# Optimization experiments

Measured on AMD Instinct MI355X. Metric: run time of the kernel, lower is better.

## Reference

```python
import jax, jax.numpy as jnp
import numpy as np

EPS = 1e-7

def _convolve(A, x, W, lw, lb):
    # A: [s,i,j,c+1] relation adjacency; keep first c=4 relations
    Ar = A[..., :-1]                               # [s,i,j,c]
    norm = 1.0 / (jnp.sum(Ar, axis=2) + EPS)       # [s,i,c]
    A_new = Ar * norm[:, :, None, :]               # [s,i,j,c]
    # contract neighbors first to avoid the [s,i,j,a,b] Theta tensor;
    # same math: x_new[s,i,b] = sum_{j,a,c} x[s,j,a] W[a,b,c] A_new[s,i,j,c]
    M = jnp.einsum('sijc,sja->siac', A_new, x)     # [s,i,a,c]
    return jnp.einsum('siac,abc->sib', M, W) + x @ lw + lb

def setup_inputs() -> dict:
    key = jax.random.key(0)
    ks = jax.random.split(key, 20)
    bz, n, cin = 512, 128, 32
    h1, h2, h3, h4, nrel = 64, 64, 128, 64, 4
    xavier = lambda k, shape: jax.random.uniform(k, shape, jnp.float32, -1.0, 1.0) * np.sqrt(6.0 / (shape[0] + shape[1]))
    return {
        'A': jax.random.uniform(ks[0], (bz, n, n, nrel + 1), jnp.float32),
        'x': jax.random.normal(ks[1], (bz, n, cin), jnp.float32),
        'conv1_w': xavier(ks[2], (cin, h1, nrel)),
        'conv1_lw': xavier(ks[3], (cin, h1)),
        'conv1_lb': jnp.zeros((h1,), jnp.float32),
        'conv2_w': xavier(ks[4], (h1 + cin, h2, nrel)),
        'conv2_lw': xavier(ks[5], (h1 + cin, h2)),
        'conv2_lb': jnp.zeros((h2,), jnp.float32),
        'gate_w': xavier(ks[6], (h2 + cin, 1)),
        'gate_b': jnp.zeros((1,), jnp.float32),
        'nn_w': xavier(ks[7], (h2 + cin, h3)),
        'nn_b': jnp.zeros((h3,), jnp.float32),
        'lin3_w': xavier(ks[8], (h3, h3)),
        'lin3_b': jnp.zeros((h3,), jnp.float32),
        'lin4_w': xavier(ks[9], (h3, h4)),
        'lin4_b': jnp.zeros((h4,), jnp.float32),
        'lin5_w': xavier(ks[10], (h4, 1)),
        'lin5_b': jnp.zeros((1,), jnp.float32),
    }

def reference(A, x, conv1_w, conv1_lw, conv1_lb, conv2_w, conv2_lw, conv2_lb,
              gate_w, gate_b, nn_w, nn_b, lin3_w, lin3_b, lin4_w, lin4_b, lin5_w, lin5_b):
    # dropout is identity in eval mode (drop_out=0.0)
    h1 = jnp.tanh(_convolve(A, x, conv1_w, conv1_lw, conv1_lb))            # [s,n,h1]
    h2 = jnp.tanh(_convolve(A, jnp.concatenate([h1, x], -1), conv2_w, conv2_lw, conv2_lb))
    xc = jnp.concatenate([h2, x], -1)                                      # [s,n,h2+cin]
    # GlobalAttention pooling: softmax of gate over nodes of each graph
    gate = jax.nn.softmax(xc @ gate_w + gate_b, axis=1)                    # [s,n,1]
    out = jnp.tanh(xc @ nn_w + nn_b)                                       # [s,n,h3]
    pooled = jnp.sum(gate * out, axis=1)                                   # [s,h3]
    h3 = jnp.tanh(pooled)
    h4 = jnp.tanh(h3 @ lin3_w + lin3_b)
    h5 = jnp.tanh(h4 @ lin4_w + lin4_b)
    return jax.nn.sigmoid(h5 @ lin5_w + lin5_b)                            # [s,1]
```

## Files before the change

kernel.cpp:

```cpp
#include <hip/hip_runtime.h>
#include <math.h>

#define SN  512
#define NN  128
#define CIN 32
#define CA  5
#define HH  64
#define YY  96
#define H3  128
#define H4  64
#define EPSF 1e-7f

typedef __attribute__((ext_vector_type(8))) short  bf16x8;
typedef __attribute__((ext_vector_type(4))) float  f32x4;
typedef __attribute__((ext_vector_type(4))) unsigned short us4;

#define MFMA16 __builtin_amdgcn_mfma_f32_16x16x32_bf16

__device__ inline unsigned short f2b(float f) {
    unsigned u = __builtin_bit_cast(unsigned, f);
    return (unsigned short)((u + 0x7FFFu + ((u >> 16) & 1u)) >> 16);
}
__device__ inline float b2f(unsigned short h) {
    unsigned u = ((unsigned)h) << 16;
    return __builtin_bit_cast(float, u);
}
__device__ inline bf16x8 pack8(float4 f0, float4 f1) {
    bf16x8 v;
    v[0]=(short)f2b(f0.x); v[1]=(short)f2b(f0.y); v[2]=(short)f2b(f0.z); v[3]=(short)f2b(f0.w);
    v[4]=(short)f2b(f1.x); v[5]=(short)f2b(f1.y); v[6]=(short)f2b(f1.z); v[7]=(short)f2b(f1.w);
    return v;
}
__device__ inline bf16x8 scale8(bf16x8 a, float s) {
    bf16x8 o;
    #pragma unroll
    for (int q = 0; q < 8; ++q)
        o[q] = (short)f2b(b2f((unsigned short)a[q]) * s);
    return o;
}
__device__ inline bf16x8 load_xfrag(const float* xg, int row, int kg) {
    float4 f0 = *(const float4*)(xg + row*CIN + kg*8);
    float4 f1 = *(const float4*)(xg + row*CIN + kg*8 + 4);
    return pack8(f0, f1);
}

__device__ inline void pz_store4(short* PZ, int row, int colsh, const f32x4& pc) {
    int byo = (colsh*2) ^ ((row & 7) << 4);
    us4 w;
    w[0]=f2b(pc[0]); w[1]=f2b(pc[1]); w[2]=f2b(pc[2]); w[3]=f2b(pc[3]);
    *(us4*)&PZ[row*128 + (byo >> 1)] = w;
}
__device__ inline bf16x8 pz_load8(const short* PZ, int row, int colsh) {
    int byo = (colsh*2) ^ ((row & 7) << 4);
    return *(const bf16x8*)&PZ[row*128 + (byo >> 1)];
}
__device__ inline int h1_idx(int row, int col) {
    return row*64 + ((((col >> 3) ^ (row & 7)) << 3) | (col & 7));
}

__global__ __launch_bounds__(512) void pack_weights(
    const float* __restrict__ w1, const float* __restrict__ lw1,
    const float* __restrict__ w2, const float* __restrict__ lw2,
    const float* __restrict__ nw, unsigned short* __restrict__ wp)
{
    int t = blockIdx.x*512 + threadIdx.x;
    if (t < 10240) {
        int c = t >> 11, rem = t & 2047, b = rem >> 5, a = rem & 31;
        float v = (c < 4) ? w1[(a*64+b)*4 + c] : lw1[a*64+b];
        wp[t] = f2b(v);
    } else if (t < 40960) {
        int u = t - 10240;
        int c = u / 6144, rem = u % 6144, b = rem / 96, a = rem % 96;
        float v = (c < 4) ? w2[(a*64+b)*4 + c] : lw2[a*64+b];
        wp[t] = f2b(v);
    } else {
        int u = t - 40960;
        int b = u / 96, a = u % 96;
        wp[t] = f2b(nw[a*128 + b]);
    }
}

template<int CINY>
__device__ __forceinline__ void conv_core(
    const unsigned short* __restrict__ wp, const float* __restrict__ LB,
    short* PZ, short* H1, bf16x8 xfrag,
    const bf16x8 (&Af)[4][4], int wave, int lm, int kg)
{
    constexpr int K32  = CINY / 32;
    constexpr int WOFF = (CINY == 32) ? 0 : 10240;
    const int jrow = wave*16 + lm;

    f32x4 acc[4];
    #pragma unroll
    for (int n = 0; n < 4; ++n) acc[n] = (f32x4){0.f,0.f,0.f,0.f};

    #pragma unroll
    for (int ks = 0; ks < K32; ++ks) {
        bf16x8 yk;
        if constexpr (CINY == 32) yk = xfrag;
        else yk = (ks == 0) ? *(const bf16x8*)&H1[h1_idx(jrow, kg*8)]
               : (ks == 1) ? *(const bf16x8*)&H1[h1_idx(jrow, 32 + kg*8)]
               : xfrag;
        #pragma unroll
        for (int n = 0; n < 4; ++n) {
            const bf16x8 bw = *(const bf16x8*)&wp[WOFF + (4*64 + n*16+lm)*CINY + ks*32 + kg*8];
            acc[n] = MFMA16(yk, bw, acc[n], 0,0,0);
        }
    }
    #pragma unroll
    for (int c = 0; c < 4; ++c) {
        f32x4 pc[4];
        #pragma unroll
        for (int n = 0; n < 4; ++n) pc[n] = (f32x4){0.f,0.f,0.f,0.f};
        #pragma unroll
        for (int ks = 0; ks < K32; ++ks) {
            bf16x8 yk;
            if constexpr (CINY == 32) yk = xfrag;
            else yk = (ks == 0) ? *(const bf16x8*)&H1[h1_idx(jrow, kg*8)]
                   : (ks == 1) ? *(const bf16x8*)&H1[h1_idx(jrow, 32 + kg*8)]
                   : xfrag;
            #pragma unroll
            for (int n = 0; n < 4; ++n) {
                const bf16x8 bw = *(const bf16x8*)&wp[WOFF + (c*64 + n*16+lm)*CINY + ks*32 + kg*8];
                pc[n] = MFMA16(yk, bw, pc[n], 0,0,0);
            }
        }
        #pragma unroll
        for (int n = 0; n < 4; ++n)
            pz_store4(PZ, c*64 + n*16+lm, wave*16 + kg*4, pc[n]);
    }
    __syncthreads();

    #pragma unroll
    for (int jt = 0; jt < 4; ++jt) {
        #pragma unroll
        for (int c = 0; c < 4; ++c) {
            #pragma unroll
            for (int n = 0; n < 4; ++n) {
                const bf16x8 bp = pz_load8(PZ, c*64 + n*16+lm, jt*32 + kg*8);
                acc[n] = MFMA16(Af[jt][c], bp, acc[n], 0,0,0);
            }
        }
    }

    #pragma unroll
    for (int n = 0; n < 4; ++n) {
        const float lbv = LB[n*16 + lm];
        #pragma unroll
        for (int r = 0; r < 4; ++r)
            H1[h1_idx(wave*16 + kg*4 + r, n*16 + lm)] = (short)f2b(tanhf(lbv + acc[n][r]));
    }
    __syncthreads();
}

__global__ __launch_bounds__(512, 4) void fused_kernel(
    const float* __restrict__ A, const float* __restrict__ x,
    const unsigned short* __restrict__ wp,
    const float* __restrict__ lb1, const float* __restrict__ lb2,
    const float* __restrict__ gw, const float* __restrict__ gb,
    const float* __restrict__ nb,
    const float* __restrict__ l3w, const float* __restrict__ l3b,
    const float* __restrict__ l4w, const float* __restrict__ l4b,
    const float* __restrict__ l5w, const float* __restrict__ l5b,
    float* __restrict__ out)
{
    __shared__ __align__(16) char smem[81920];
    short* PZ = (short*)smem;
    short* H1 = (short*)(smem + 65536);
    short* xcb40 = (short*)smem;
    float* part = (float*)(smem + 10240);
    float* gate = (float*)(smem + 14336);
    float* red  = (float*)(smem + 14848);
    float* tmpv = (float*)(smem + 15360);

    const int s = blockIdx.x, tid = threadIdx.x;
    const int wave = tid>>6, lane = tid&63, lm = lane&15, kg = lane>>4;
    const float* xg = x + (size_t)s*NN*CIN;

    bf16x8 Af[4][4];
    {
        short* scr = PZ + wave*2688;
        const float* Ab = A + ((size_t)(s*NN + wave*16))*NN*CA;
        const int r8 = lane>>3, l8 = lane&7;
        float sm[2][4];
        #pragma unroll
        for (int rh = 0; rh < 2; ++rh)
            #pragma unroll
            for (int c = 0; c < 4; ++c) sm[rh][c] = 0.f;

        #pragma unroll
        for (int jt = 0; jt < 4; ++jt) {
            #pragma unroll
            for (int rh = 0; rh < 2; ++rh) {
                const int r = r8 + rh*8;
                const float* rp = Ab + (size_t)r*(NN*CA) + jt*160 + l8*20;
                float4 q0 = *(const float4*)(rp);
                float4 q1 = *(const float4*)(rp+4);
                float4 q2 = *(const float4*)(rp+8);
                float4 q3 = *(const float4*)(rp+12);
                float4 q4 = *(const float4*)(rp+16);
                short* lr = scr + r*168;
                const int jb = 4*l8;
                lr[0*40 + jb+0] = (short)f2b(q0.x);
                lr[1*40 + jb+0] = (short)f2b(q0.y);
                lr[2*40 + jb+0] = (short)f2b(q0.z);
                lr[3*40 + jb+0] = (short)f2b(q0.w);
                lr[0*40 + jb+1] = (short)f2b(q1.y);
                lr[1*40 + jb+1] = (short)f2b(q1.z);
                lr[2*40 + jb+1] = (short)f2b(q1.w);
                lr[3*40 + jb+1] = (short)f2b(q2.x);
                lr[0*40 + jb+2] = (short)f2b(q2.z);
                lr[1*40 + jb+2] = (short)f2b(q2.w);
                lr[2*40 + jb+2] = (short)f2b(q3.x);
                lr[3*40 + jb+2] = (short)f2b(q3.y);
                lr[0*40 + jb+3] = (short)f2b(q3.w);
                lr[1*40 + jb+3] = (short)f2b(q4.x);
                lr[2*40 + jb+3] = (short)f2b(q4.y);
                lr[3*40 + jb+3] = (short)f2b(q4.z);
                sm[rh][0] += q0.x + q1.y + q2.z + q3.w;
                sm[rh][1] += q0.y + q1.z + q2.w + q4.x;
                sm[rh][2] += q0.z + q1.w + q3.x + q4.y;
                sm[rh][3] += q0.w + q2.x + q3.y + q4.z;
            }
            #pragma unroll
            for (int c = 0; c < 4; ++c)
                Af[jt][c] = *(const bf16x8*)&scr[lm*168 + c*40 + kg*8];
        }
        #pragma unroll
        for (int off = 1; off < 8; off <<= 1) {
            #pragma unroll
            for (int rh = 0; rh < 2; ++rh)
                #pragma unroll
                for (int c = 0; c < 4; ++c)
                    sm[rh][c] += __shfl_xor(sm[rh][c], off);
        }
        float* invL = (float*)scr;
        if (l8 == 0) {
            #pragma unroll
            for (int rh = 0; rh < 2; ++rh)
                #pragma unroll
                for (int c = 0; c < 4; ++c)
                    invL[(r8 + rh*8)*4 + c] = 1.0f/(sm[rh][c] + EPSF);
        }
        const f32x4 iv = *(const f32x4*)&invL[lm*4];
        #pragma unroll
        for (int jt = 0; jt < 4; ++jt)
            #pragma unroll
            for (int c = 0; c < 4; ++c)
                Af[jt][c] = scale8(Af[jt][c], iv[c]);
    }
    __syncthreads();

    const bf16x8 xfrag = load_xfrag(xg, wave*16 + lm, kg);

    conv_core<CIN>(wp, lb1, PZ, H1, xfrag, Af, wave, lm, kg);

    conv_core<YY>(wp, lb2, PZ, H1, xfrag, Af, wave, lm, kg);

    for (int t = tid; t < NN*CIN; t += 512)
        xcb40[(t>>5)*40 + (t&31)] = (short)f2b(xg[t]);
    __syncthreads();

    {
        const int i = tid >> 2, t4 = tid & 3;
        float z = 0.f;
        #pragma unroll
        for (int q = 0; q < 16; ++q) {
            const int a = t4*16 + q;
            z += b2f((unsigned short)H1[h1_idx(i, a)]) * gw[a];
        }
        #pragma unroll
        for (int q = 0; q < 8; ++q) {
            const int a = t4*8 + q;
            z += b2f((unsigned short)xcb40[i*40 + a]) * gw[64 + a];
        }
        z += __shfl_xor(z, 1); z += __shfl_xor(z, 2);
        if (t4 == 0) red[i] = z + gb[0];
    }
    __syncthreads();
    if (wave == 0) {
        float v0 = red[lane], v1 = red[lane + 64];
        float m = fmaxf(v0, v1);
        #pragma unroll
        for (int off = 32; off > 0; off >>= 1) m = fmaxf(m, __shfl_xor(m, off));
        float e0 = expf(v0 - m), e1 = expf(v1 - m);
        float ssum = e0 + e1;
        #pragma unroll
        for (int off = 32; off > 0; off >>= 1) ssum += __shfl_xor(ssum, off);
        gate[lane] = e0 / ssum; gate[lane + 64] = e1 / ssum;
    }
    __syncthreads();

    {
        f32x4 pacc[8];
        #pragma unroll
        for (int nt = 0; nt < 8; ++nt) pacc[nt] = (f32x4){0.f,0.f,0.f,0.f};
        const int arow = wave*16 + lm;
        #pragma unroll
        for (int ks = 0; ks < 3; ++ks) {
            bf16x8 afp;
            if (ks == 0)      afp = *(const bf16x8*)&H1[h1_idx(arow, kg*8)];
            else if (ks == 1) afp = *(const bf16x8*)&H1[h1_idx(arow, 32 + kg*8)];
            else              afp = *(const bf16x8*)&xcb40[arow*40 + kg*8];
            #pragma unroll
            for (int nt = 0; nt < 8; ++nt) {
                const bf16x8 bfp = *(const bf16x8*)&wp[40960 + (nt*16+lm)*96 + ks*32 + kg*8];
                pacc[nt] = MFMA16(afp, bfp, pacc[nt], 0,0,0);
            }
        }
        #pragma unroll
        for (int nt = 0; nt < 8; ++nt) {
            const float nbv = nb[nt*16+lm];
            float pv = 0.f;
            #pragma unroll
            for (int r = 0; r < 4; ++r)
                pv += gate[wave*16 + kg*4 + r] * tanhf(pacc[nt][r] + nbv);
            pv += __shfl_xor(pv, 16);
            pv += __shfl_xor(pv, 32);
            if (lane < 16) part[wave*128 + nt*16 + lm] = pv;
        }
    }
    __syncthreads();
    if (tid < H3) {
        float pooled = 0.f;
        #pragma unroll
        for (int w = 0; w < 8; ++w) pooled += part[w*128 + tid];
        tmpv[tid] = tanhf(pooled);
    }
    __syncthreads();
    if (tid < H3) {
        float a4 = l3b[tid];
        for (int aa = 0; aa < H3; ++aa) a4 += tmpv[aa] * l3w[aa*H3 + tid];
        red[tid] = tanhf(a4);
    }
    __syncthreads();
    if (tid < H4) {
        float a5 = l4b[tid];
        for (int aa = 0; aa < H3; ++aa) a5 += red[aa] * l4w[aa*H4 + tid];
        gate[tid] = tanhf(a5);
    }
    __syncthreads();
    if (tid == 0) {
        float zo = l5b[0];
        for (int aa = 0; aa < H4; ++aa) zo += gate[aa] * l5w[aa];
        out[s] = 1.0f / (1.0f + expf(-zo));
    }
}

extern "C" void kernel_launch(void* const* d_in, const int* in_sizes, int n_in,
                              void* d_out, int out_size, void* d_ws, size_t ws_size,
                              hipStream_t stream)
{
    const float* A   = (const float*)d_in[0];
    const float* x   = (const float*)d_in[1];
    const float* w1  = (const float*)d_in[2];
    const float* lw1 = (const float*)d_in[3];
    const float* lb1 = (const float*)d_in[4];
    const float* w2  = (const float*)d_in[5];
    const float* lw2 = (const float*)d_in[6];
    const float* lb2 = (const float*)d_in[7];
    const float* gw  = (const float*)d_in[8];
    const float* gb  = (const float*)d_in[9];
    const float* nw  = (const float*)d_in[10];
    const float* nb  = (const float*)d_in[11];
    const float* l3w = (const float*)d_in[12];
    const float* l3b = (const float*)d_in[13];
    const float* l4w = (const float*)d_in[14];
    const float* l4b = (const float*)d_in[15];
    const float* l5w = (const float*)d_in[16];
    const float* l5b = (const float*)d_in[17];
    float* out = (float*)d_out;
    unsigned short* wp = (unsigned short*)d_ws;

    pack_weights<<<104, 512, 0, stream>>>(w1, lw1, w2, lw2, nw, wp);
    fused_kernel<<<SN, 512, 0, stream>>>(A, x, wp, lb1, lb2, gw, gb, nb,
                                         l3w, l3b, l4w, l4b, l5w, l5b, out);
}
```

Measured before the change: 90.78 us.

## Spill normalized adjacency fragments to global scratch instead of holding in registers

The 16 bf16x8 adjacency fragments (64 VGPRs per lane) are no longer kept in registers across both conv stages. A is now read twice: a first pass computes the row sums, and a second pass writes pre-normalized bf16 values through LDS, then out to a per-block global scratch buffer. Each conv stage reloads the fragments from that buffer, which frees registers and folds the normalization into the conversion. The cost is a second read of A and extra global writes and reads of 128KB per block, with a larger workspace needed.

```diff
diff --git a/kernel.cpp b/kernel.cpp
--- a/kernel.cpp
+++ b/kernel.cpp
@@ -30,13 +30,6 @@
     v[0]=(short)f2b(f0.x); v[1]=(short)f2b(f0.y); v[2]=(short)f2b(f0.z); v[3]=(short)f2b(f0.w);
     v[4]=(short)f2b(f1.x); v[5]=(short)f2b(f1.y); v[6]=(short)f2b(f1.z); v[7]=(short)f2b(f1.w);
     return v;
-}
-__device__ inline bf16x8 scale8(bf16x8 a, float s) {
-    bf16x8 o;
-    #pragma unroll
-    for (int q = 0; q < 8; ++q)
-        o[q] = (short)f2b(b2f((unsigned short)a[q]) * s);
-    return o;
 }
 __device__ inline bf16x8 load_xfrag(const float* xg, int row, int kg) {
     float4 f0 = *(const float4*)(xg + row*CIN + kg*8);
@@ -84,7 +77,8 @@
 __device__ __forceinline__ void conv_core(
     const unsigned short* __restrict__ wp, const float* __restrict__ LB,
     short* PZ, short* H1, bf16x8 xfrag,
-    const bf16x8 (&Af)[4][4], int wave, int lm, int kg)
+    const unsigned short* __restrict__ pkw,
+    int wave, int lane, int lm, int kg)
 {
     constexpr int K32  = CINY / 32;
     constexpr int WOFF = (CINY == 32) ? 0 : 10240;
@@ -135,10 +129,11 @@
     for (int jt = 0; jt < 4; ++jt) {
         #pragma unroll
         for (int c = 0; c < 4; ++c) {
+            const bf16x8 afr = *(const bf16x8*)&pkw[(size_t)((jt*4 + c)*64 + lane)*8];
             #pragma unroll
             for (int n = 0; n < 4; ++n) {
                 const bf16x8 bp = pz_load8(PZ, c*64 + n*16+lm, jt*32 + kg*8);
-                acc[n] = MFMA16(Af[jt][c], bp, acc[n], 0,0,0);
+                acc[n] = MFMA16(afr, bp, acc[n], 0,0,0);
             }
         }
     }
@@ -156,6 +151,7 @@
 __global__ __launch_bounds__(512, 4) void fused_kernel(
     const float* __restrict__ A, const float* __restrict__ x,
     const unsigned short* __restrict__ wp,
+    unsigned short* __restrict__ pk,
     const float* __restrict__ lb1, const float* __restrict__ lb2,
     const float* __restrict__ gw, const float* __restrict__ gb,
     const float* __restrict__ nb,
@@ -176,8 +172,8 @@
     const int s = blockIdx.x, tid = threadIdx.x;
     const int wave = tid>>6, lane = tid&63, lm = lane&15, kg = lane>>4;
     const float* xg = x + (size_t)s*NN*CIN;
-
-    bf16x8 Af[4][4];
+    unsigned short* pkw = pk + (size_t)s*65536 + wave*8192;
+
     {
         short* scr = PZ + wave*2688;
         const float* Ab = A + ((size_t)(s*NN + wave*16))*NN*CA;
@@ -187,6 +183,38 @@
         for (int rh = 0; rh < 2; ++rh)
             #pragma unroll
             for (int c = 0; c < 4; ++c) sm[rh][c] = 0.f;
+
+        #pragma unroll
+        for (int jt = 0; jt < 4; ++jt) {
+            #pragma unroll
+            for (int rh = 0; rh < 2; ++rh) {
+                const int r = r8 + rh*8;
+                const float* rp = Ab + (size_t)r*(NN*CA) + jt*160 + l8*20;
+                float4 q0 = *(const float4*)(rp);
+                float4 q1 = *(const float4*)(rp+4);
+                float4 q2 = *(const float4*)(rp+8);
+                float4 q3 = *(const float4*)(rp+12);
+                float4 q4 = *(const float4*)(rp+16);
+                sm[rh][0] += q0.x + q1.y + q2.z + q3.w;
+                sm[rh][1] += q0.y + q1.z + q2.w + q4.x;
+                sm[rh][2] += q0.z + q1.w + q3.x + q4.y;
+                sm[rh][3] += q0.w + q2.x + q3.y + q4.z;
+            }
+        }
+        #pragma unroll
+        for (int off = 1; off < 8; off <<= 1) {
+            #pragma unroll
+            for (int rh = 0; rh < 2; ++rh)
+                #pragma unroll
+                for (int c = 0; c < 4; ++c)
+                    sm[rh][c] += __shfl_xor(sm[rh][c], off);
+        }
+        float iv[2][4];
+        #pragma unroll
+        for (int rh = 0; rh < 2; ++rh)
+            #pragma unroll
+            for (int c = 0; c < 4; ++c)
+                iv[rh][c] = 1.0f/(sm[rh][c] + EPSF);
 
         #pragma unroll
         for (int jt = 0; jt < 4; ++jt) {
@@ -201,61 +229,37 @@
                 float4 q4 = *(const float4*)(rp+16);
                 short* lr = scr + r*168;
                 const int jb = 4*l8;
-                lr[0*40 + jb+0] = (short)f2b(q0.x);
-                lr[1*40 + jb+0] = (short)f2b(q0.y);
-                lr[2*40 + jb+0] = (short)f2b(q0.z);
-                lr[3*40 + jb+0] = (short)f2b(q0.w);
-                lr[0*40 + jb+1] = (short)f2b(q1.y);
-                lr[1*40 + jb+1] = (short)f2b(q1.z);
-                lr[2*40 + jb+1] = (short)f2b(q1.w);
-                lr[3*40 + jb+1] = (short)f2b(q2.x);
-                lr[0*40 + jb+2] = (short)f2b(q2.z);
-                lr[1*40 + jb+2] = (short)f2b(q2.w);
-                lr[2*40 + jb+2] = (short)f2b(q3.x);
-                lr[3*40 + jb+2] = (short)f2b(q3.y);
-                lr[0*40 + jb+3] = (short)f2b(q3.w);
-                lr[1*40 + jb+3] = (short)f2b(q4.x);
-                lr[2*40 + jb+3] = (short)f2b(q4.y);
-                lr[3*40 + jb+3] = (short)f2b(q4.z);
-                sm[rh][0] += q0.x + q1.y + q2.z + q3.w;
-                sm[rh][1] += q0.y + q1.z + q2.w + q4.x;
-                sm[rh][2] += q0.z + q1.w + q3.x + q4.y;
-                sm[rh][3] += q0.w + q2.x + q3.y + q4.z;
-            }
-            #pragma unroll
-            for (int c = 0; c < 4; ++c)
-                Af[jt][c] = *(const bf16x8*)&scr[lm*168 + c*40 + kg*8];
-        }
-        #pragma unroll
-        for (int off = 1; off < 8; off <<= 1) {
-            #pragma unroll
-            for (int rh = 0; rh < 2; ++rh)
-                #pragma unroll
-                for (int c = 0; c < 4; ++c)
-                    sm[rh][c] += __shfl_xor(sm[rh][c], off);
-        }
-        float* invL = (float*)scr;
-        if (l8 == 0) {
-            #pragma unroll
-            for (int rh = 0; rh < 2; ++rh)
-                #pragma unroll
-                for (int c = 0; c < 4; ++c)
-                    invL[(r8 + rh*8)*4 + c] = 1.0f/(sm[rh][c] + EPSF);
-        }
-        const f32x4 iv = *(const f32x4*)&invL[lm*4];
-        #pragma unroll
-        for (int jt = 0; jt < 4; ++jt)
-            #pragma unroll
-            for (int c = 0; c < 4; ++c)
-                Af[jt][c] = scale8(Af[jt][c], iv[c]);
+                lr[0*40 + jb+0] = (short)f2b(q0.x * iv[rh][0]);
+                lr[1*40 + jb+0] = (short)f2b(q0.y * iv[rh][1]);
+                lr[2*40 + jb+0] = (short)f2b(q0.z * iv[rh][2]);
+                lr[3*40 + jb+0] = (short)f2b(q0.w * iv[rh][3]);
+                lr[0*40 + jb+1] = (short)f2b(q1.y * iv[rh][0]);
+                lr[1*40 + jb+1] = (short)f2b(q1.z * iv[rh][1]);
+                lr[2*40 + jb+1] = (short)f2b(q1.w * iv[rh][2]);
+                lr[3*40 + jb+1] = (short)f2b(q2.x * iv[rh][3]);
+                lr[0*40 + jb+2] = (short)f2b(q2.z * iv[rh][0]);
+                lr[1*40 + jb+2] = (short)f2b(q2.w * iv[rh][1]);
+                lr[2*40 + jb+2] = (short)f2b(q3.x * iv[rh][2]);
+                lr[3*40 + jb+2] = (short)f2b(q3.y * iv[rh][3]);
+                lr[0*40 + jb+3] = (short)f2b(q3.w * iv[rh][0]);
+                lr[1*40 + jb+3] = (short)f2b(q4.x * iv[rh][1]);
+                lr[2*40 + jb+3] = (short)f2b(q4.y * iv[rh][2]);
+                lr[3*40 + jb+3] = (short)f2b(q4.z * iv[rh][3]);
+            }
+            #pragma unroll
+            for (int c = 0; c < 4; ++c) {
+                const bf16x8 fr = *(const bf16x8*)&scr[lm*168 + c*40 + kg*8];
+                *(bf16x8*)&pkw[(size_t)((jt*4 + c)*64 + lane)*8] = fr;
+            }
+        }
     }
     __syncthreads();
 
     const bf16x8 xfrag = load_xfrag(xg, wave*16 + lm, kg);
 
-    conv_core<CIN>(wp, lb1, PZ, H1, xfrag, Af, wave, lm, kg);
-
-    conv_core<YY>(wp, lb2, PZ, H1, xfrag, Af, wave, lm, kg);
+    conv_core<CIN>(wp, lb1, PZ, H1, xfrag, pkw, wave, lane, lm, kg);
+
+    conv_core<YY>(wp, lb2, PZ, H1, xfrag, pkw, wave, lane, lm, kg);
 
     for (int t = tid; t < NN*CIN; t += 512)
         xcb40[(t>>5)*40 + (t&31)] = (short)f2b(xg[t]);
@@ -371,8 +375,9 @@
     const float* l5b = (const float*)d_in[17];
     float* out = (float*)d_out;
     unsigned short* wp = (unsigned short*)d_ws;
+    unsigned short* pk = (unsigned short*)((char*)d_ws + 131072);
 
     pack_weights<<<104, 512, 0, stream>>>(w1, lw1, w2, lw2, nw, wp);
-    fused_kernel<<<SN, 512, 0, stream>>>(A, x, wp, lb1, lb2, gw, gb, nb,
+    fused_kernel<<<SN, 512, 0, stream>>>(A, x, wp, pk, lb1, lb2, gw, gb, nb,
                                          l3w, l3b, l4w, l4b, l5w, l5b, out);
 }
```

Result: slower. 194.5 us (+114.2%).

## Stream normalized adjacency tiles through LDS per conv stage instead of register-resident A

Applied to the files above, without the earlier changes.

Replaces the per-wave register-resident normalized adjacency fragments with a row-sum pre-pass followed by per-j-tile streaming of A from global memory into LDS in each conv stage, interleaved with computing the matching projection tile. This reduces register pressure and LDS footprint (no full 256x128 projection buffer). In exchange, A is read from global memory three times instead of once, and each tile iteration adds two block barriers.

```diff
diff --git a/kernel.cpp b/kernel.cpp
--- a/kernel.cpp
+++ b/kernel.cpp
@@ -31,28 +31,18 @@
     v[4]=(short)f2b(f1.x); v[5]=(short)f2b(f1.y); v[6]=(short)f2b(f1.z); v[7]=(short)f2b(f1.w);
     return v;
 }
-__device__ inline bf16x8 scale8(bf16x8 a, float s) {
-    bf16x8 o;
-    #pragma unroll
-    for (int q = 0; q < 8; ++q)
-        o[q] = (short)f2b(b2f((unsigned short)a[q]) * s);
-    return o;
-}
 __device__ inline bf16x8 load_xfrag(const float* xg, int row, int kg) {
     float4 f0 = *(const float4*)(xg + row*CIN + kg*8);
     float4 f1 = *(const float4*)(xg + row*CIN + kg*8 + 4);
     return pack8(f0, f1);
 }
-
-__device__ inline void pz_store4(short* PZ, int row, int colsh, const f32x4& pc) {
-    int byo = (colsh*2) ^ ((row & 7) << 4);
-    us4 w;
-    w[0]=f2b(pc[0]); w[1]=f2b(pc[1]); w[2]=f2b(pc[2]); w[3]=f2b(pc[3]);
-    *(us4*)&PZ[row*128 + (byo >> 1)] = w;
-}
-__device__ inline bf16x8 pz_load8(const short* PZ, int row, int colsh) {
-    int byo = (colsh*2) ^ ((row & 7) << 4);
-    return *(const bf16x8*)&PZ[row*128 + (byo >> 1)];
+__device__ inline bf16x8 lds_load8(const short* L, int idx) {
+    us4 lo = *(const us4*)&L[idx];
+    us4 hi = *(const us4*)&L[idx + 4];
+    bf16x8 v;
+    v[0]=(short)lo[0]; v[1]=(short)lo[1]; v[2]=(short)lo[2]; v[3]=(short)lo[3];
+    v[4]=(short)hi[0]; v[5]=(short)hi[1]; v[6]=(short)hi[2]; v[7]=(short)hi[3];
+    return v;
 }
 __device__ inline int h1_idx(int row, int col) {
     return row*64 + ((((col >> 3) ^ (row & 7)) << 3) | (col & 7));
@@ -81,74 +71,102 @@
 }
 
 template<int CINY>
-__device__ __forceinline__ void conv_core(
+__device__ __forceinline__ void conv_stage(
     const unsigned short* __restrict__ wp, const float* __restrict__ LB,
-    short* PZ, short* H1, bf16x8 xfrag,
-    const bf16x8 (&Af)[4][4], int wave, int lm, int kg)
+    short* AS, short* PS, short* H1,
+    const float* __restrict__ xg, const float* __restrict__ Ag,
+    const float iv[4], int wave, int lm, int kg, int tid)
 {
     constexpr int K32  = CINY / 32;
     constexpr int WOFF = (CINY == 32) ? 0 : 10240;
-    const int jrow = wave*16 + lm;
+    const int r = tid >> 2, q = tid & 3;
+    const int cp = wave >> 1, jj = wave & 1;
 
     f32x4 acc[4];
     #pragma unroll
     for (int n = 0; n < 4; ++n) acc[n] = (f32x4){0.f,0.f,0.f,0.f};
 
-    #pragma unroll
-    for (int ks = 0; ks < K32; ++ks) {
-        bf16x8 yk;
-        if constexpr (CINY == 32) yk = xfrag;
-        else yk = (ks == 0) ? *(const bf16x8*)&H1[h1_idx(jrow, kg*8)]
-               : (ks == 1) ? *(const bf16x8*)&H1[h1_idx(jrow, 32 + kg*8)]
-               : xfrag;
-        #pragma unroll
-        for (int n = 0; n < 4; ++n) {
-            const bf16x8 bw = *(const bf16x8*)&wp[WOFF + (4*64 + n*16+lm)*CINY + ks*32 + kg*8];
-            acc[n] = MFMA16(yk, bw, acc[n], 0,0,0);
-        }
-    }
-    #pragma unroll
-    for (int c = 0; c < 4; ++c) {
-        f32x4 pc[4];
-        #pragma unroll
-        for (int n = 0; n < 4; ++n) pc[n] = (f32x4){0.f,0.f,0.f,0.f};
+    {
+        const int irow = wave*16 + lm;
+        const bf16x8 yx = load_xfrag(xg, irow, kg);
         #pragma unroll
         for (int ks = 0; ks < K32; ++ks) {
             bf16x8 yk;
-            if constexpr (CINY == 32) yk = xfrag;
-            else yk = (ks == 0) ? *(const bf16x8*)&H1[h1_idx(jrow, kg*8)]
-                   : (ks == 1) ? *(const bf16x8*)&H1[h1_idx(jrow, 32 + kg*8)]
-                   : xfrag;
+            if constexpr (CINY == 32) yk = yx;
+            else yk = (ks == 0) ? lds_load8(H1, h1_idx(irow, kg*8))
+                   : (ks == 1) ? lds_load8(H1, h1_idx(irow, 32 + kg*8))
+                   : yx;
             #pragma unroll
             for (int n = 0; n < 4; ++n) {
-                const bf16x8 bw = *(const bf16x8*)&wp[WOFF + (c*64 + n*16+lm)*CINY + ks*32 + kg*8];
-                pc[n] = MFMA16(yk, bw, pc[n], 0,0,0);
-            }
-        }
-        #pragma unroll
-        for (int n = 0; n < 4; ++n)
-            pz_store4(PZ, c*64 + n*16+lm, wave*16 + kg*4, pc[n]);
-    }
-    __syncthreads();
-
-    #pragma unroll
+                const bf16x8 bw = *(const bf16x8*)&wp[WOFF + (4*64 + n*16+lm)*CINY + ks*32 + kg*8];
+                acc[n] = MFMA16(yk, bw, acc[n], 0,0,0);
+            }
+        }
+    }
+
     for (int jt = 0; jt < 4; ++jt) {
+        {
+            const float* rp = Ag + (size_t)r*(NN*CA) + (jt*32 + q*8)*5;
+            #pragma unroll
+            for (int g2 = 0; g2 < 2; ++g2) {
+                const float* p = rp + g2*20;
+                float4 q0 = *(const float4*)(p);
+                float4 q1 = *(const float4*)(p+4);
+                float4 q2 = *(const float4*)(p+8);
+                float4 q3 = *(const float4*)(p+12);
+                float4 q4 = *(const float4*)(p+16);
+                const int j0 = q*8 + g2*4;
+                us4 w;
+                w[0]=f2b(q0.x*iv[0]); w[1]=f2b(q1.y*iv[0]); w[2]=f2b(q2.z*iv[0]); w[3]=f2b(q3.w*iv[0]);
+                *(us4*)&AS[(0*128 + r)*36 + j0] = w;
+                w[0]=f2b(q0.y*iv[1]); w[1]=f2b(q1.z*iv[1]); w[2]=f2b(q2.w*iv[1]); w[3]=f2b(q4.x*iv[1]);
+                *(us4*)&AS[(1*128 + r)*36 + j0] = w;
+                w[0]=f2b(q0.z*iv[2]); w[1]=f2b(q1.w*iv[2]); w[2]=f2b(q3.x*iv[2]); w[3]=f2b(q4.y*iv[2]);
+                *(us4*)&AS[(2*128 + r)*36 + j0] = w;
+                w[0]=f2b(q0.w*iv[3]); w[1]=f2b(q2.x*iv[3]); w[2]=f2b(q3.y*iv[3]); w[3]=f2b(q4.z*iv[3]);
+                *(us4*)&AS[(3*128 + r)*36 + j0] = w;
+            }
+        }
+        {
+            const int jrow = jt*32 + jj*16 + lm;
+            const bf16x8 yx = load_xfrag(xg, jrow, kg);
+            #pragma unroll
+            for (int n = 0; n < 4; ++n) {
+                f32x4 pc = (f32x4){0.f,0.f,0.f,0.f};
+                #pragma unroll
+                for (int ks = 0; ks < K32; ++ks) {
+                    bf16x8 yk;
+                    if constexpr (CINY == 32) yk = yx;
+                    else yk = (ks == 0) ? lds_load8(H1, h1_idx(jrow, kg*8))
+                           : (ks == 1) ? lds_load8(H1, h1_idx(jrow, 32 + kg*8))
+                           : yx;
+                    const bf16x8 bw = *(const bf16x8*)&wp[WOFF + (cp*64 + n*16+lm)*CINY + ks*32 + kg*8];
+                    pc = MFMA16(yk, bw, pc, 0,0,0);
+                }
+                us4 w;
+                w[0]=f2b(pc[0]); w[1]=f2b(pc[1]); w[2]=f2b(pc[2]); w[3]=f2b(pc[3]);
+                *(us4*)&PS[(cp*64 + n*16+lm)*36 + jj*16 + kg*4] = w;
+            }
+        }
+        __syncthreads();
         #pragma unroll
         for (int c = 0; c < 4; ++c) {
+            const bf16x8 af = lds_load8(AS, (c*128 + wave*16+lm)*36 + kg*8);
             #pragma unroll
             for (int n = 0; n < 4; ++n) {
-                const bf16x8 bp = pz_load8(PZ, c*64 + n*16+lm, jt*32 + kg*8);
-                acc[n] = MFMA16(Af[jt][c], bp, acc[n], 0,0,0);
-            }
-        }
+                const bf16x8 bp = lds_load8(PS, (c*64 + n*16+lm)*36 + kg*8);
+                acc[n] = MFMA16(af, bp, acc[n], 0,0,0);
+            }
+        }
+        __syncthreads();
     }
 
     #pragma unroll
     for (int n = 0; n < 4; ++n) {
         const float lbv = LB[n*16 + lm];
         #pragma unroll
-        for (int r = 0; r < 4; ++r)
-            H1[h1_idx(wave*16 + kg*4 + r, n*16 + lm)] = (short)f2b(tanhf(lbv + acc[n][r]));
+        for (int rr = 0; rr < 4; ++rr)
+            H1[h1_idx(wave*16 + kg*4 + rr, n*16 + lm)] = (short)f2b(tanhf(lbv + acc[n][rr]));
     }
     __syncthreads();
 }
@@ -164,9 +182,10 @@
     const float* __restrict__ l5w, const float* __restrict__ l5b,
     float* __restrict__ out)
 {
-    __shared__ __align__(16) char smem[81920];
-    short* PZ = (short*)smem;
-    short* H1 = (short*)(smem + 65536);
+    __shared__ __align__(16) char smem[71680];
+    short* AS = (short*)smem;
+    short* PS = (short*)(smem + 36864);
+    short* H1 = (short*)(smem + 55296);
     short* xcb40 = (short*)smem;
     float* part = (float*)(smem + 10240);
     float* gate = (float*)(smem + 14336);
@@ -176,86 +195,37 @@
     const int s = blockIdx.x, tid = threadIdx.x;
     const int wave = tid>>6, lane = tid&63, lm = lane&15, kg = lane>>4;
     const float* xg = x + (size_t)s*NN*CIN;
-
-    bf16x8 Af[4][4];
+    const float* Ag = A + (size_t)s*NN*NN*CA;
+
+    float iv[4];
     {
-        short* scr = PZ + wave*2688;
-        const float* Ab = A + ((size_t)(s*NN + wave*16))*NN*CA;
-        const int r8 = lane>>3, l8 = lane&7;
-        float sm[2][4];
-        #pragma unroll
-        for (int rh = 0; rh < 2; ++rh)
-            #pragma unroll
-            for (int c = 0; c < 4; ++c) sm[rh][c] = 0.f;
-
-        #pragma unroll
-        for (int jt = 0; jt < 4; ++jt) {
-            #pragma unroll
-            for (int rh = 0; rh < 2; ++rh) {
-                const int r = r8 + rh*8;
-                const float* rp = Ab + (size_t)r*(NN*CA) + jt*160 + l8*20;
-                float4 q0 = *(const float4*)(rp);
-                float4 q1 = *(const float4*)(rp+4);
-                float4 q2 = *(const float4*)(rp+8);
-                float4 q3 = *(const float4*)(rp+12);
-                float4 q4 = *(const float4*)(rp+16);
-                short* lr = scr + r*168;
-                const int jb = 4*l8;
-                lr[0*40 + jb+0] = (short)f2b(q0.x);
-                lr[1*40 + jb+0] = (short)f2b(q0.y);
-                lr[2*40 + jb+0] = (short)f2b(q0.z);
-                lr[3*40 + jb+0] = (short)f2b(q0.w);
-                lr[0*40 + jb+1] = (short)f2b(q1.y);
-                lr[1*40 + jb+1] = (short)f2b(q1.z);
-                lr[2*40 + jb+1] = (short)f2b(q1.w);
-                lr[3*40 + jb+1] = (short)f2b(q2.x);
-                lr[0*40 + jb+2] = (short)f2b(q2.z);
-                lr[1*40 + jb+2] = (short)f2b(q2.w);
-                lr[2*40 + jb+2] = (short)f2b(q3.x);
-                lr[3*40 + jb+2] = (short)f2b(q3.y);
-                lr[0*40 + jb+3] = (short)f2b(q3.w);
-                lr[1*40 + jb+3] = (short)f2b(q4.x);
-                lr[2*40 + jb+3] = (short)f2b(q4.y);
-                lr[3*40 + jb+3] = (short)f2b(q4.z);
-                sm[rh][0] += q0.x + q1.y + q2.z + q3.w;
-                sm[rh][1] += q0.y + q1.z + q2.w + q4.x;
-                sm[rh][2] += q0.z + q1.w + q3.x + q4.y;
-                sm[rh][3] += q0.w + q2.x + q3.y + q4.z;
-            }
-            #pragma unroll
-            for (int c = 0; c < 4; ++c)
-                Af[jt][c] = *(const bf16x8*)&scr[lm*168 + c*40 + kg*8];
-        }
-        #pragma unroll
-        for (int off = 1; off < 8; off <<= 1) {
-            #pragma unroll
-            for (int rh = 0; rh < 2; ++rh)
-                #pragma unroll
-                for (int c = 0; c < 4; ++c)
-                    sm[rh][c] += __shfl_xor(sm[rh][c], off);
-        }
-        float* invL = (float*)scr;
-        if (l8 == 0) {
-            #pragma unroll
-            for (int rh = 0; rh < 2; ++rh)
-                #pragma unroll
-                for (int c = 0; c < 4; ++c)
-                    invL[(r8 + rh*8)*4 + c] = 1.0f/(sm[rh][c] + EPSF);
-        }
-        const f32x4 iv = *(const f32x4*)&invL[lm*4];
-        #pragma unroll
-        for (int jt = 0; jt < 4; ++jt)
-            #pragma unroll
-            for (int c = 0; c < 4; ++c)
-                Af[jt][c] = scale8(Af[jt][c], iv[c]);
-    }
-    __syncthreads();
-
-    const bf16x8 xfrag = load_xfrag(xg, wave*16 + lm, kg);
-
-    conv_core<CIN>(wp, lb1, PZ, H1, xfrag, Af, wave, lm, kg);
-
-    conv_core<YY>(wp, lb2, PZ, H1, xfrag, Af, wave, lm, kg);
+        const int r = tid >> 2, q = tid & 3;
+        const float* rp = Ag + (size_t)r*(NN*CA) + q*160;
+        float s0=0.f, s1=0.f, s2=0.f, s3=0.f;
+        #pragma unroll
+        for (int g = 0; g < 8; ++g) {
+            const float* p = rp + g*20;
+            float4 q0 = *(const float4*)(p);
+            float4 q1 = *(const float4*)(p+4);
+            float4 q2 = *(const float4*)(p+8);
+            float4 q3 = *(const float4*)(p+12);
+            float4 q4 = *(const float4*)(p+16);
+            s0 += q0.x + q1.y + q2.z + q3.w;
+            s1 += q0.y + q1.z + q2.w + q4.x;
+            s2 += q0.z + q1.w + q3.x + q4.y;
+            s3 += q0.w + q2.x + q3.y + q4.z;
+        }
+        s0 += __shfl_xor(s0, 1); s0 += __shfl_xor(s0, 2);
+        s1 += __shfl_xor(s1, 1); s1 += __shfl_xor(s1, 2);
+        s2 += __shfl_xor(s2, 1); s2 += __shfl_xor(s2, 2);
+        s3 += __shfl_xor(s3, 1); s3 += __shfl_xor(s3, 2);
+        iv[0] = 1.0f/(s0 + EPSF); iv[1] = 1.0f/(s1 + EPSF);
+        iv[2] = 1.0f/(s2 + EPSF); iv[3] = 1.0f/(s3 + EPSF);
+    }
+
+    conv_stage<CIN>(wp, lb1, AS, PS, H1, xg, Ag, iv, wave, lm, kg, tid);
+
+    conv_stage<YY>(wp, lb2, AS, PS, H1, xg, Ag, iv, wave, lm, kg, tid);
 
     for (int t = tid; t < NN*CIN; t += 512)
         xcb40[(t>>5)*40 + (t&31)] = (short)f2b(xg[t]);
@@ -265,13 +235,13 @@
         const int i = tid >> 2, t4 = tid & 3;
         float z = 0.f;
         #pragma unroll
-        for (int q = 0; q < 16; ++q) {
-            const int a = t4*16 + q;
+        for (int qq = 0; qq < 16; ++qq) {
+            const int a = t4*16 + qq;
             z += b2f((unsigned short)H1[h1_idx(i, a)]) * gw[a];
         }
         #pragma unroll
-        for (int q = 0; q < 8; ++q) {
-            const int a = t4*8 + q;
+        for (int qq = 0; qq < 8; ++qq) {
+            const int a = t4*8 + qq;
             z += b2f((unsigned short)xcb40[i*40 + a]) * gw[64 + a];
         }
         z += __shfl_xor(z, 1); z += __shfl_xor(z, 2);
@@ -299,8 +269,8 @@
         #pragma unroll
         for (int ks = 0; ks < 3; ++ks) {
             bf16x8 afp;
-            if (ks == 0)      afp = *(const bf16x8*)&H1[h1_idx(arow, kg*8)];
-            else if (ks == 1) afp = *(const bf16x8*)&H1[h1_idx(arow, 32 + kg*8)];
+            if (ks == 0)      afp = lds_load8(H1, h1_idx(arow, kg*8));
+            else if (ks == 1) afp = lds_load8(H1, h1_idx(arow, 32 + kg*8));
             else              afp = *(const bf16x8*)&xcb40[arow*40 + kg*8];
             #pragma unroll
             for (int nt = 0; nt < 8; ++nt) {
@@ -313,8 +283,8 @@
             const float nbv = nb[nt*16+lm];
             float pv = 0.f;
             #pragma unroll
-            for (int r = 0; r < 4; ++r)
-                pv += gate[wave*16 + kg*4 + r] * tanhf(pacc[nt][r] + nbv);
+            for (int rr = 0; rr < 4; ++rr)
+                pv += gate[wave*16 + kg*4 + rr] * tanhf(pacc[nt][rr] + nbv);
             pv += __shfl_xor(pv, 16);
             pv += __shfl_xor(pv, 32);
             if (lane < 16) part[wave*128 + nt*16 + lm] = pv;
```

Result: slower. 128.3 us (+41.4%).
